# Optimization experiments

Measured on AMD Instinct MI355X. Metric: run time of the kernel, lower is better.

## Reference

```python
import jax, jax.numpy as jnp
import numpy as np

B, T, D, H, O = 512, 512, 256, 200, 1


def setup_inputs() -> dict:
    key = jax.random.key(0)
    ks = jax.random.split(key, 7)
    s = 1.0 / np.sqrt(H)  # PyTorch LSTM init scale
    x = jax.random.normal(ks[0], (B, T, D), dtype=jnp.float32)
    W_ih = jax.random.uniform(ks[1], (4 * H, D), jnp.float32, -s, s)
    W_hh = jax.random.uniform(ks[2], (4 * H, H), jnp.float32, -s, s)
    b_ih = jax.random.uniform(ks[3], (4 * H,), jnp.float32, -s, s)
    b_hh = jax.random.uniform(ks[4], (4 * H,), jnp.float32, -s, s)
    so = 1.0 / np.sqrt(H * T)
    W_out = jax.random.uniform(ks[5], (O, H * T), jnp.float32, -so, so)
    b_out = jax.random.uniform(ks[6], (O,), jnp.float32, -so, so)
    return {"input_seq": x, "W_ih": W_ih, "W_hh": W_hh, "b_ih": b_ih,
            "b_hh": b_hh, "W_out": W_out, "b_out": b_out}


def _lstm(x, W_ih, W_hh, b_ih, b_hh):
    # Precompute input contribution for all timesteps: [B,T,4H] -> [T,B,4H]
    pre = jnp.einsum('btd,gd->btg', x, W_ih) + b_ih + b_hh
    pre = jnp.transpose(pre, (1, 0, 2))
    h0 = jnp.zeros((x.shape[0], H), x.dtype)
    c0 = jnp.zeros((x.shape[0], H), x.dtype)

    def step(carry, pt):
        h, c = carry
        gates = pt + h @ W_hh.T  # [B,4H]
        i, f, g, o = jnp.split(gates, 4, axis=-1)  # PyTorch gate order i,f,g,o
        i = jax.nn.sigmoid(i)
        f = jax.nn.sigmoid(f)
        g = jnp.tanh(g)
        o = jax.nn.sigmoid(o)
        c_new = f * c + i * g
        h_new = o * jnp.tanh(c_new)
        return (h_new, c_new), h_new

    _, outs = jax.lax.scan(step, (h0, c0), pre)  # outs: [T,B,H]
    return jnp.transpose(outs, (1, 0, 2))  # [B,T,H]


def reference(input_seq, W_ih, W_hh, b_ih, b_hh, W_out, b_out):
    all_outs = _lstm(input_seq, W_ih, W_hh, b_ih, b_hh)  # [B,T,H]
    flat = all_outs.reshape(all_outs.shape[0], -1)  # [B, T*H]
    return flat @ W_out.T + b_out  # [B, O]
```

## Files before the change

### kernel.cpp

```cpp
#include <hip/hip_runtime.h>
#include <hip/hip_bf16.h>

#define B_SZ 512
#define T_SZ 512
#define D_SZ 256
#define H_SZ 200
#define G4   800
#define NSUB 50
#define GST8 808
#define GDUMP (2*GST8)
#define HTS  232
#define BS   8

typedef __attribute__((ext_vector_type(8))) short short8;
typedef __attribute__((ext_vector_type(4))) short short4v;
typedef __attribute__((ext_vector_type(4))) float f32x4;

__device__ __forceinline__ unsigned short f2bf(float x) {
    unsigned u = __builtin_bit_cast(unsigned, x);
    unsigned r = (u + 0x7FFFu + ((u >> 16) & 1u)) >> 16;
    return (unsigned short)r;
}
__device__ __forceinline__ float sigm(float v) { return 1.f / (1.f + __expf(-v)); }

__device__ __forceinline__ void gl_lds16(const void* g, void* l) {
    __builtin_amdgcn_global_load_lds(
        (const __attribute__((address_space(1))) unsigned int*)g,
        (__attribute__((address_space(3))) unsigned int*)l, 16, 0, 0);
}

__global__ __launch_bounds__(256)
void cvt_bf16(const float* __restrict__ src, unsigned short* __restrict__ dst, int n4)
{
    int i = blockIdx.x * 256 + threadIdx.x;
    const int stride = gridDim.x * 256;
    for (; i < n4; i += stride) {
        float4 v = ((const float4*)src)[i];
        unsigned a = (unsigned)f2bf(v.x) | ((unsigned)f2bf(v.y) << 16);
        unsigned b = (unsigned)f2bf(v.z) | ((unsigned)f2bf(v.w) << 16);
        ((uint2*)dst)[i] = make_uint2(a, b);
    }
}

__global__ __launch_bounds__(256)
void pre_gemm(const unsigned short* __restrict__ xbf,
              const unsigned short* __restrict__ wbf,
              const float* __restrict__ bih, const float* __restrict__ bhh,
              unsigned short* __restrict__ pre, int t0)
{
    const int tt = blockIdx.x;
    const int t  = t0 + tt;
    const int b0 = blockIdx.y * 64;
    const int g0 = blockIdx.z * 256;

    __shared__ unsigned short Al[256 * 32];
    __shared__ unsigned short Bl[64 * 32];

    const int tid  = threadIdx.x;
    const int w    = tid >> 6;
    const int lane = tid & 63;
    const int col  = lane & 15, q = lane >> 4;

    f32x4 acc[4][4];
    #pragma unroll
    for (int i = 0; i < 4; ++i)
        #pragma unroll
        for (int j = 0; j < 4; ++j) acc[i][j] = (f32x4)0.f;

    const int arow = w * 64 + (lane >> 2);
    const int akoff = (lane & 3) * 8;
    const int brow = b0 + w * 16 + (lane >> 2);

    for (int kc = 0; kc < 8; ++kc) {
        const int d0 = kc * 32;
        if (kc) __syncthreads();
        #pragma unroll
        for (int j = 0; j < 4; ++j) {
            int g = g0 + arow + j * 16;
            if (g > G4 - 1) g = G4 - 1;
            gl_lds16(wbf + (size_t)g * D_SZ + d0 + akoff,
                     (void*)(Al + (w * 64 + j * 16) * 32));
        }
        gl_lds16(xbf + ((size_t)brow * T_SZ + t) * D_SZ + d0 + akoff,
                 (void*)(Bl + (w * 16) * 32));
        __syncthreads();

        short8 af[4], bv[4];
        #pragma unroll
        for (int s = 0; s < 4; ++s)
            af[s] = *(const short8*)&Al[(w * 64 + s * 16 + col) * 32 + q * 8];
        #pragma unroll
        for (int s = 0; s < 4; ++s)
            bv[s] = *(const short8*)&Bl[(s * 16 + col) * 32 + q * 8];
        #pragma unroll
        for (int gs = 0; gs < 4; ++gs)
            #pragma unroll
            for (int bs = 0; bs < 4; ++bs)
                acc[gs][bs] = __builtin_amdgcn_mfma_f32_16x16x32_bf16(af[gs], bv[bs], acc[gs][bs], 0, 0, 0);
    }

    #pragma unroll
    for (int gs = 0; gs < 4; ++gs) {
        const int S = blockIdx.z * 16 + w * 4 + gs;
        if (S < NSUB) {
            const int gq = S * 16 + q * 4;
            const float4 bi = *(const float4*)&bih[gq];
            const float4 bh = *(const float4*)&bhh[gq];
            #pragma unroll
            for (int bs = 0; bs < 4; ++bs) {
                f32x4 a = acc[gs][bs];
                unsigned lo = (unsigned)f2bf(a[0] + bi.x + bh.x) |
                              ((unsigned)f2bf(a[1] + bi.y + bh.y) << 16);
                unsigned hi = (unsigned)f2bf(a[2] + bi.z + bh.z) |
                              ((unsigned)f2bf(a[3] + bi.w + bh.w) << 16);
                const size_t idx = (((size_t)tt * NSUB + S) * 4 + q) * 512 + (b0 + bs * 16 + col);
                ((uint2*)pre)[idx] = make_uint2(lo, hi);
            }
        }
    }
}

__global__ __launch_bounds__(512, 2)
void lstm_rec(const unsigned short* __restrict__ pre,
              const float* __restrict__ Whh,
              const float* __restrict__ Wout,
              const float* __restrict__ bout,
              float* __restrict__ state,
              float* __restrict__ out,
              int t0, int C_T)
{
    const int bk = blockIdx.x;
    const int cidx = (bk >> 3) + (bk & 7) * 32;
    const int b0 = cidx * 2;

    const int tid = threadIdx.x, lane = tid & 63, wv = tid >> 6;
    const int col = lane & 15, q = lane >> 4;

    __shared__ __align__(16) unsigned short preS[2 * BS * 1600];
    __shared__ __align__(16) float gates[2 * GST8 + 256];
    __shared__ __align__(16) short hT[3 * HTS];
    __shared__ float redbuf[8];

    const int tbase = (wv < 2) ? wv * 7 : 14 + (wv - 2) * 6;

    int gaddr[7], pofs[7], tjv[7];
    #pragma unroll
    for (int j = 0; j < 7; ++j) {
        const int tr = tbase + j;
        const int tj = tr > 49 ? 49 : tr;
        tjv[j] = tj;
        const bool valid = (tr <= 49) && (col < 2);
        gaddr[j] = valid ? (col * GST8 + tj * 16 + q * 4) : (GDUMP + lane * 4);
        pofs[j]  = (tj * 4 + q) * 8 + (col & 1) * 4;
    }

    short8 aw[7][6];
#if __has_builtin(__builtin_amdgcn_mfma_f32_16x16x16bf16_1k)
    short4v aw6[7];
#else
    short8 aw6[7];
#endif
    #pragma unroll
    for (int j = 0; j < 7; ++j) {
        const int g = tjv[j] * 16 + col;
        const float* wr = Whh + (size_t)g * H_SZ;
        #pragma unroll
        for (int kc = 0; kc < 6; ++kc) {
            const int k = kc * 32 + q * 8;
            float4 f0 = *(const float4*)(wr + k);
            float4 f1 = *(const float4*)(wr + k + 4);
            short8 s;
            s[0] = (short)f2bf(f0.x); s[1] = (short)f2bf(f0.y);
            s[2] = (short)f2bf(f0.z); s[3] = (short)f2bf(f0.w);
            s[4] = (short)f2bf(f1.x); s[5] = (short)f2bf(f1.y);
            s[6] = (short)f2bf(f1.z); s[7] = (short)f2bf(f1.w);
            aw[j][kc] = s;
        }
#if __has_builtin(__builtin_amdgcn_mfma_f32_16x16x16bf16_1k)
        short4v t4 = (short4v)0;
        if (q < 2) {
            float4 f = *(const float4*)(wr + 192 + q * 4);
            t4[0] = (short)f2bf(f.x); t4[1] = (short)f2bf(f.y);
            t4[2] = (short)f2bf(f.z); t4[3] = (short)f2bf(f.w);
        }
        aw6[j] = t4;
#else
        short8 t8 = (short8)0;
        if (q == 0) {
            float4 f0 = *(const float4*)(wr + 192);
            float4 f1 = *(const float4*)(wr + 196);
            t8[0] = (short)f2bf(f0.x); t8[1] = (short)f2bf(f0.y);
            t8[2] = (short)f2bf(f0.z); t8[3] = (short)f2bf(f0.w);
            t8[4] = (short)f2bf(f1.x); t8[5] = (short)f2bf(f1.y);
            t8[6] = (short)f2bf(f1.z); t8[7] = (short)f2bf(f1.w);
        }
        aw6[j] = t8;
#endif
    }

    float* h_st  = state;
    float* c_st  = state + (size_t)B_SZ * H_SZ;
    float* oa_st = state + (size_t)2 * B_SZ * H_SZ;

    for (int i = tid; i < 3 * HTS; i += 512) {
        const int r = i / HTS, k = i - r * HTS;
        short v = 0;
        if (t0 > 0 && r < 2 && k < H_SZ) v = (short)f2bf(h_st[(size_t)(b0 + r) * H_SZ + k]);
        hT[i] = v;
    }

    const int n_ew = tid >> 8;
    const int h_ew = tid & 255;
    const bool ewv = (h_ew < H_SZ);
    float c_v = 0.f, oa_v = 0.f, wpf0 = 0.f, wpf1 = 0.f;
    if (ewv) {
        wpf0 = Wout[(size_t)t0 * H_SZ + h_ew];
        const int t1 = (t0 + 1 < T_SZ) ? t0 + 1 : T_SZ - 1;
        wpf1 = Wout[(size_t)t1 * H_SZ + h_ew];
        if (t0 > 0) {
            c_v  = c_st [(size_t)(b0 + n_ew) * H_SZ + h_ew];
            oa_v = oa_st[(size_t)(b0 + n_ew) * H_SZ + h_ew];
        }
    }

    const int nblk = C_T / BS;
    const char* preb = (const char*)pre;

    {
        const char* src = preb + ((size_t)wv * 200) * 4096 + (size_t)b0 * 8;
        unsigned short* dst = preS + (0 * BS + wv) * 1600;
        gl_lds16(src + (size_t)lane * 4096,         dst);
        gl_lds16(src + (size_t)(lane + 64) * 4096,  dst + 512);
        gl_lds16(src + (size_t)(lane + 128) * 4096, dst + 1024);
        gl_lds16(src + (size_t)(lane + 136) * 4096, dst + 1088);
    }
    __syncthreads();

    const short* hrow = hT + (col < 2 ? col : 2) * HTS;

    for (int blk = 0; blk < nblk; ++blk) {
        const int bn = blk & 1;
        {
            const int nb = (blk + 1 < nblk) ? blk + 1 : blk;
            const char* src = preb + ((size_t)(nb * BS + wv) * 200) * 4096 + (size_t)b0 * 8;
            unsigned short* dst = preS + ((bn ^ 1) * BS + wv) * 1600;
            gl_lds16(src + (size_t)lane * 4096,         dst);
            gl_lds16(src + (size_t)(lane + 64) * 4096,  dst + 512);
            gl_lds16(src + (size_t)(lane + 128) * 4096, dst + 1024);
            gl_lds16(src + (size_t)(lane + 136) * 4096, dst + 1088);
        }
        const unsigned short* psb = preS + bn * (BS * 1600);

        for (int s = 0; s < BS; ++s) {
            const int tc = blk * BS + s;
            const unsigned short* ps = psb + s * 1600;

            f32x4 acc[7];
            #pragma unroll
            for (int j = 0; j < 7; ++j) {
                const uint2 p = *(const uint2*)(ps + pofs[j]);
                f32x4 a;
                a[0] = __builtin_bit_cast(float, p.x << 16);
                a[1] = __builtin_bit_cast(float, p.x & 0xFFFF0000u);
                a[2] = __builtin_bit_cast(float, p.y << 16);
                a[3] = __builtin_bit_cast(float, p.y & 0xFFFF0000u);
                acc[j] = a;
            }
            #pragma unroll
            for (int kc = 0; kc < 6; ++kc) {
                const short8 bf = *(const short8*)(hrow + kc * 32 + q * 8);
                #pragma unroll
                for (int j = 0; j < 7; ++j)
                    acc[j] = __builtin_amdgcn_mfma_f32_16x16x32_bf16(aw[j][kc], bf, acc[j], 0, 0, 0);
            }
#if __has_builtin(__builtin_amdgcn_mfma_f32_16x16x16bf16_1k)
            {
                const short4v bt = *(const short4v*)(hrow + 192 + q * 4);
                #pragma unroll
                for (int j = 0; j < 7; ++j)
                    acc[j] = __builtin_amdgcn_mfma_f32_16x16x16bf16_1k(aw6[j], bt, acc[j], 0, 0, 0);
            }
#else
            {
                const short8 bt = *(const short8*)(hrow + 192 + q * 8);
                #pragma unroll
                for (int j = 0; j < 7; ++j)
                    acc[j] = __builtin_amdgcn_mfma_f32_16x16x32_bf16(aw6[j], bt, acc[j], 0, 0, 0);
            }
#endif
            #pragma unroll
            for (int j = 0; j < 7; ++j)
                *(f32x4*)&gates[gaddr[j]] = acc[j];
            __syncthreads();

            if (ewv) {
                const int gb = n_ew * GST8 + h_ew;
                const float gi = sigm(gates[gb]);
                const float gf = sigm(gates[gb + 200]);
                const float gg = 2.f * sigm(2.f * gates[gb + 400]) - 1.f;
                const float go = sigm(gates[gb + 600]);
                const float cn = gf * c_v + gi * gg;
                c_v = cn;
                const float hv = go * (2.f * sigm(2.f * cn) - 1.f);
                oa_v += hv * wpf0;
                wpf0 = wpf1;
                const int tn = (t0 + tc + 2 < T_SZ) ? t0 + tc + 2 : T_SZ - 1;
                wpf1 = Wout[(size_t)tn * H_SZ + h_ew];
                hT[n_ew * HTS + h_ew] = (short)f2bf(hv);
                if (t0 + C_T < T_SZ && tc == C_T - 1)
                    h_st[(size_t)(b0 + n_ew) * H_SZ + h_ew] = hv;
            }
            __syncthreads();
        }
    }

    if (t0 + C_T >= T_SZ) {
        float v = oa_v;
        #pragma unroll
        for (int off = 32; off; off >>= 1) v += __shfl_down(v, off);
        if (lane == 0) redbuf[wv] = v;
        __syncthreads();
        if (tid < 2)
            out[b0 + tid] = redbuf[tid * 4] + redbuf[tid * 4 + 1] +
                            redbuf[tid * 4 + 2] + redbuf[tid * 4 + 3] + bout[0];
    } else if (ewv) {
        c_st [(size_t)(b0 + n_ew) * H_SZ + h_ew] = c_v;
        oa_st[(size_t)(b0 + n_ew) * H_SZ + h_ew] = oa_v;
    }
}

extern "C" void kernel_launch(void* const* d_in, const int* in_sizes, int n_in,
                              void* d_out, int out_size, void* d_ws, size_t ws_size,
                              hipStream_t stream)
{
    const float* x    = (const float*)d_in[0];
    const float* Wih  = (const float*)d_in[1];
    const float* Whh  = (const float*)d_in[2];
    const float* bih  = (const float*)d_in[3];
    const float* bhh  = (const float*)d_in[4];
    const float* Wout = (const float*)d_in[5];
    const float* bout = (const float*)d_in[6];
    float* out = (float*)d_out;

    char* ws = (char*)d_ws;
    float* state = (float*)ws;
    size_t off = (size_t)3 * B_SZ * H_SZ * sizeof(float);
    unsigned short* xbf = (unsigned short*)(ws + off);
    off += (size_t)B_SZ * T_SZ * D_SZ * 2;
    unsigned short* wbf = (unsigned short*)(ws + off);
    off += (size_t)G4 * D_SZ * 2;
    unsigned short* pre = (unsigned short*)(ws + off);

    const size_t per_t = (size_t)NSUB * 4 * 512 * 4 * 2;
    int ct = 512;
    while (ct > BS && off + (size_t)ct * per_t > ws_size) ct >>= 1;

    cvt_bf16<<<dim3(2048), dim3(256), 0, stream>>>(x, xbf, B_SZ * T_SZ * D_SZ / 4);
    cvt_bf16<<<dim3(64),   dim3(256), 0, stream>>>(Wih, wbf, G4 * D_SZ / 4);

    for (int t0 = 0; t0 < T_SZ; t0 += ct) {
        pre_gemm<<<dim3(ct, 8, 4), dim3(256), 0, stream>>>(
            xbf, wbf, bih, bhh, pre, t0);
        lstm_rec<<<dim3(256), dim3(512), 0, stream>>>(
            pre, Whh, Wout, bout, state, out, t0, ct);
    }
}
```

Measured before the change: 1.872 ms.

## Stage bf16 Wout in LDS, skip dead MFMA tile, hoist h fragment loads

Wout is converted to bf16 in a new pre-pass and double-buffered into LDS through global_load_lds alongside the pre-activation blocks. This replaces the per-step global register prefetch inside the elementwise phase. Waves that own only six gate tiles now skip the seventh (clamped, duplicate) MFMA chain, and only lanes with col<2 store to the gates buffer, so the dump region is removed. The h fragments are loaded once per step before the MFMA loops, and the chunk-boundary h store moves to the end of the kernel. Wout is now read at bf16 precision, which adds a small rounding error to the output projection.

```diff
diff --git a/kernel.cpp b/kernel.cpp
--- a/kernel.cpp
+++ b/kernel.cpp
@@ -8,7 +8,6 @@
 #define G4   800
 #define NSUB 50
 #define GST8 808
-#define GDUMP (2*GST8)
 #define HTS  232
 #define BS   8
 
@@ -20,6 +19,9 @@
     unsigned u = __builtin_bit_cast(unsigned, x);
     unsigned r = (u + 0x7FFFu + ((u >> 16) & 1u)) >> 16;
     return (unsigned short)r;
+}
+__device__ __forceinline__ float bf2f(unsigned short s) {
+    return __builtin_bit_cast(float, (unsigned)s << 16);
 }
 __device__ __forceinline__ float sigm(float v) { return 1.f / (1.f + __expf(-v)); }
 
@@ -123,7 +125,7 @@
 __global__ __launch_bounds__(512, 2)
 void lstm_rec(const unsigned short* __restrict__ pre,
               const float* __restrict__ Whh,
-              const float* __restrict__ Wout,
+              const unsigned short* __restrict__ woutbf,
               const float* __restrict__ bout,
               float* __restrict__ state,
               float* __restrict__ out,
@@ -137,20 +139,20 @@
     const int col = lane & 15, q = lane >> 4;
 
     __shared__ __align__(16) unsigned short preS[2 * BS * 1600];
-    __shared__ __align__(16) float gates[2 * GST8 + 256];
+    __shared__ __align__(16) unsigned short woutS[2 * BS * 200];
+    __shared__ __align__(16) float gates[2 * GST8];
     __shared__ __align__(16) short hT[3 * HTS];
     __shared__ float redbuf[8];
 
-    const int tbase = (wv < 2) ? wv * 7 : 14 + (wv - 2) * 6;
-
-    int gaddr[7], pofs[7], tjv[7];
+    const bool w7 = (wv < 2);
+    const int tbase = w7 ? wv * 7 : 14 + (wv - 2) * 6;
+
+    int gaddr[7], pofs[7];
     #pragma unroll
     for (int j = 0; j < 7; ++j) {
         const int tr = tbase + j;
         const int tj = tr > 49 ? 49 : tr;
-        tjv[j] = tj;
-        const bool valid = (tr <= 49) && (col < 2);
-        gaddr[j] = valid ? (col * GST8 + tj * 16 + q * 4) : (GDUMP + lane * 4);
+        gaddr[j] = col * GST8 + tj * 16 + q * 4;
         pofs[j]  = (tj * 4 + q) * 8 + (col & 1) * 4;
     }
 
@@ -162,7 +164,8 @@
 #endif
     #pragma unroll
     for (int j = 0; j < 7; ++j) {
-        const int g = tjv[j] * 16 + col;
+        const int tr = tbase + j;
+        const int g = (tr > 49 ? 49 : tr) * 16 + col;
         const float* wr = Whh + (size_t)g * H_SZ;
         #pragma unroll
         for (int kc = 0; kc < 6; ++kc) {
@@ -212,15 +215,10 @@
     const int n_ew = tid >> 8;
     const int h_ew = tid & 255;
     const bool ewv = (h_ew < H_SZ);
-    float c_v = 0.f, oa_v = 0.f, wpf0 = 0.f, wpf1 = 0.f;
-    if (ewv) {
-        wpf0 = Wout[(size_t)t0 * H_SZ + h_ew];
-        const int t1 = (t0 + 1 < T_SZ) ? t0 + 1 : T_SZ - 1;
-        wpf1 = Wout[(size_t)t1 * H_SZ + h_ew];
-        if (t0 > 0) {
-            c_v  = c_st [(size_t)(b0 + n_ew) * H_SZ + h_ew];
-            oa_v = oa_st[(size_t)(b0 + n_ew) * H_SZ + h_ew];
-        }
+    float c_v = 0.f, oa_v = 0.f, hv_last = 0.f;
+    if (ewv && t0 > 0) {
+        c_v  = c_st [(size_t)(b0 + n_ew) * H_SZ + h_ew];
+        oa_v = oa_st[(size_t)(b0 + n_ew) * H_SZ + h_ew];
     }
 
     const int nblk = C_T / BS;
@@ -228,11 +226,13 @@
 
     {
         const char* src = preb + ((size_t)wv * 200) * 4096 + (size_t)b0 * 8;
-        unsigned short* dst = preS + (0 * BS + wv) * 1600;
+        unsigned short* dst = preS + wv * 1600;
         gl_lds16(src + (size_t)lane * 4096,         dst);
         gl_lds16(src + (size_t)(lane + 64) * 4096,  dst + 512);
         gl_lds16(src + (size_t)(lane + 128) * 4096, dst + 1024);
         gl_lds16(src + (size_t)(lane + 136) * 4096, dst + 1088);
+        if (lane < 25)
+            gl_lds16(woutbf + ((size_t)(t0 + wv) * H_SZ + lane * 8), woutS + wv * 200);
     }
     __syncthreads();
 
@@ -248,16 +248,19 @@
             gl_lds16(src + (size_t)(lane + 64) * 4096,  dst + 512);
             gl_lds16(src + (size_t)(lane + 128) * 4096, dst + 1024);
             gl_lds16(src + (size_t)(lane + 136) * 4096, dst + 1088);
+            if (lane < 25)
+                gl_lds16(woutbf + ((size_t)(t0 + nb * BS + wv) * H_SZ + lane * 8),
+                         woutS + ((bn ^ 1) * BS + wv) * 200);
         }
         const unsigned short* psb = preS + bn * (BS * 1600);
+        const unsigned short* wsb = woutS + bn * (BS * 200);
 
         for (int s = 0; s < BS; ++s) {
-            const int tc = blk * BS + s;
             const unsigned short* ps = psb + s * 1600;
 
             f32x4 acc[7];
             #pragma unroll
-            for (int j = 0; j < 7; ++j) {
+            for (int j = 0; j < 6; ++j) {
                 const uint2 p = *(const uint2*)(ps + pofs[j]);
                 f32x4 a;
                 a[0] = __builtin_bit_cast(float, p.x << 16);
@@ -266,31 +269,58 @@
                 a[3] = __builtin_bit_cast(float, p.y & 0xFFFF0000u);
                 acc[j] = a;
             }
-            #pragma unroll
-            for (int kc = 0; kc < 6; ++kc) {
-                const short8 bf = *(const short8*)(hrow + kc * 32 + q * 8);
+            acc[6] = (f32x4)0.f;
+            if (w7) {
+                const uint2 p = *(const uint2*)(ps + pofs[6]);
+                f32x4 a;
+                a[0] = __builtin_bit_cast(float, p.x << 16);
+                a[1] = __builtin_bit_cast(float, p.x & 0xFFFF0000u);
+                a[2] = __builtin_bit_cast(float, p.y << 16);
+                a[3] = __builtin_bit_cast(float, p.y & 0xFFFF0000u);
+                acc[6] = a;
+            }
+
+            short8 hf[6];
+            #pragma unroll
+            for (int kc = 0; kc < 6; ++kc)
+                hf[kc] = *(const short8*)(hrow + kc * 32 + q * 8);
+#if __has_builtin(__builtin_amdgcn_mfma_f32_16x16x16bf16_1k)
+            const short4v ht_ = *(const short4v*)(hrow + 192 + q * 4);
+#else
+            const short8 ht_ = *(const short8*)(hrow + 192 + q * 8);
+#endif
+
+            #pragma unroll
+            for (int kc = 0; kc < 6; ++kc)
                 #pragma unroll
-                for (int j = 0; j < 7; ++j)
-                    acc[j] = __builtin_amdgcn_mfma_f32_16x16x32_bf16(aw[j][kc], bf, acc[j], 0, 0, 0);
-            }
-#if __has_builtin(__builtin_amdgcn_mfma_f32_16x16x16bf16_1k)
-            {
-                const short4v bt = *(const short4v*)(hrow + 192 + q * 4);
+                for (int j = 0; j < 6; ++j)
+                    acc[j] = __builtin_amdgcn_mfma_f32_16x16x32_bf16(aw[j][kc], hf[kc], acc[j], 0, 0, 0);
+#if __has_builtin(__builtin_amdgcn_mfma_f32_16x16x16bf16_1k)
+            #pragma unroll
+            for (int j = 0; j < 6; ++j)
+                acc[j] = __builtin_amdgcn_mfma_f32_16x16x16bf16_1k(aw6[j], ht_, acc[j], 0, 0, 0);
+#else
+            #pragma unroll
+            for (int j = 0; j < 6; ++j)
+                acc[j] = __builtin_amdgcn_mfma_f32_16x16x32_bf16(aw6[j], ht_, acc[j], 0, 0, 0);
+#endif
+            if (w7) {
                 #pragma unroll
-                for (int j = 0; j < 7; ++j)
-                    acc[j] = __builtin_amdgcn_mfma_f32_16x16x16bf16_1k(aw6[j], bt, acc[j], 0, 0, 0);
-            }
-#else
-            {
-                const short8 bt = *(const short8*)(hrow + 192 + q * 8);
+                for (int kc = 0; kc < 6; ++kc)
+                    acc[6] = __builtin_amdgcn_mfma_f32_16x16x32_bf16(aw[6][kc], hf[kc], acc[6], 0, 0, 0);
+#if __has_builtin(__builtin_amdgcn_mfma_f32_16x16x16bf16_1k)
+                acc[6] = __builtin_amdgcn_mfma_f32_16x16x16bf16_1k(aw6[6], ht_, acc[6], 0, 0, 0);
+#else
+                acc[6] = __builtin_amdgcn_mfma_f32_16x16x32_bf16(aw6[6], ht_, acc[6], 0, 0, 0);
+#endif
+            }
+
+            if (col < 2) {
                 #pragma unroll
-                for (int j = 0; j < 7; ++j)
-                    acc[j] = __builtin_amdgcn_mfma_f32_16x16x32_bf16(aw6[j], bt, acc[j], 0, 0, 0);
-            }
-#endif
-            #pragma unroll
-            for (int j = 0; j < 7; ++j)
-                *(f32x4*)&gates[gaddr[j]] = acc[j];
+                for (int j = 0; j < 6; ++j)
+                    *(f32x4*)&gates[gaddr[j]] = acc[j];
+                if (w7) *(f32x4*)&gates[gaddr[6]] = acc[6];
+            }
             __syncthreads();
 
             if (ewv) {
@@ -302,13 +332,9 @@
                 const float cn = gf * c_v + gi * gg;
                 c_v = cn;
                 const float hv = go * (2.f * sigm(2.f * cn) - 1.f);
-                oa_v += hv * wpf0;
-                wpf0 = wpf1;
-                const int tn = (t0 + tc + 2 < T_SZ) ? t0 + tc + 2 : T_SZ - 1;
-                wpf1 = Wout[(size_t)tn * H_SZ + h_ew];
+                oa_v += hv * bf2f(wsb[s * 200 + h_ew]);
                 hT[n_ew * HTS + h_ew] = (short)f2bf(hv);
-                if (t0 + C_T < T_SZ && tc == C_T - 1)
-                    h_st[(size_t)(b0 + n_ew) * H_SZ + h_ew] = hv;
+                hv_last = hv;
             }
             __syncthreads();
         }
@@ -324,6 +350,7 @@
             out[b0 + tid] = redbuf[tid * 4] + redbuf[tid * 4 + 1] +
                             redbuf[tid * 4 + 2] + redbuf[tid * 4 + 3] + bout[0];
     } else if (ewv) {
+        h_st [(size_t)(b0 + n_ew) * H_SZ + h_ew] = hv_last;
         c_st [(size_t)(b0 + n_ew) * H_SZ + h_ew] = c_v;
         oa_st[(size_t)(b0 + n_ew) * H_SZ + h_ew] = oa_v;
     }
@@ -349,6 +376,8 @@
     off += (size_t)B_SZ * T_SZ * D_SZ * 2;
     unsigned short* wbf = (unsigned short*)(ws + off);
     off += (size_t)G4 * D_SZ * 2;
+    unsigned short* woutbf = (unsigned short*)(ws + off);
+    off += (size_t)T_SZ * H_SZ * 2;
     unsigned short* pre = (unsigned short*)(ws + off);
 
     const size_t per_t = (size_t)NSUB * 4 * 512 * 4 * 2;
@@ -357,11 +386,12 @@
 
     cvt_bf16<<<dim3(2048), dim3(256), 0, stream>>>(x, xbf, B_SZ * T_SZ * D_SZ / 4);
     cvt_bf16<<<dim3(64),   dim3(256), 0, stream>>>(Wih, wbf, G4 * D_SZ / 4);
+    cvt_bf16<<<dim3(100),  dim3(256), 0, stream>>>(Wout, woutbf, T_SZ * H_SZ / 4);
 
     for (int t0 = 0; t0 < T_SZ; t0 += ct) {
         pre_gemm<<<dim3(ct, 8, 4), dim3(256), 0, stream>>>(
             xbf, wbf, bih, bhh, pre, t0);
         lstm_rec<<<dim3(256), dim3(512), 0, stream>>>(
-            pre, Whh, Wout, bout, state, out, t0, ct);
-    }
-}
+            pre, Whh, woutbf, bout, state, out, t0, ct);
+    }
+}
```

Result: slower. 1.942 ms (+3.7%).
